# Optimization experiments

Measured on AMD Instinct MI355X. Metric: run time of the kernel, lower is better.

The kernel has to match this reference:

```python
import jax, jax.numpy as jnp
import numpy as np

DIM = 768
HEADS = 6
HD = DIM // HEADS
B, N = 8, 4096
EPS = 1e-12  # torch F.normalize default


def setup_inputs() -> dict:
    key = jax.random.key(0)
    k1, k2, k3, k4, k5 = jax.random.split(key, 5)
    x = jax.random.normal(k1, (B, N, DIM), dtype=jnp.float32)
    y = jax.random.normal(k2, (B, N, DIM), dtype=jnp.float32)
    W_qkv = jax.random.normal(k3, (DIM, 2 * DIM), dtype=jnp.float32) * (1.0 / np.sqrt(DIM))
    temperature = jnp.ones((HEADS, 1, 1), dtype=jnp.float32)
    W_proj = jax.random.normal(k4, (DIM, DIM), dtype=jnp.float32) * (1.0 / np.sqrt(DIM))
    b_proj = jax.random.normal(k5, (DIM,), dtype=jnp.float32) * 0.01
    return {"x": x, "y": y, "W_qkv": W_qkv, "temperature": temperature,
            "W_proj": W_proj, "b_proj": b_proj}


def _l2norm(t):
    # F.normalize(dim=-1): v / max(||v||, eps)
    n = jnp.sqrt(jnp.sum(t * t, axis=-1, keepdims=True))
    return t / jnp.maximum(n, EPS)


def reference(x, y, W_qkv, temperature, W_proj, b_proj):
    Bx, Nx, C = x.shape
    # qkv: [B,N,2C] -> [B,N,2,H,hd] -> q,k: [B,H,hd,N]
    qkv = (x @ W_qkv).reshape(Bx, Nx, 2, HEADS, HD)
    qkv = jnp.transpose(qkv, (2, 0, 3, 4, 1))  # [2,B,H,hd,N]
    q, k = qkv[0], qkv[1]
    # v: [B,H,hd,N]
    v = jnp.transpose(y.reshape(Bx, Nx, HEADS, HD), (0, 2, 3, 1))
    q = _l2norm(q)  # normalize over token dim N
    k = _l2norm(k)
    # channel-channel attention: [B,H,hd,hd]
    attn = jnp.einsum('bhcn,bhdn->bhcd', q, k) * temperature
    attn = jax.nn.softmax(attn, axis=-1)
    out = jnp.einsum('bhcd,bhdn->bhcn', attn, v)  # [B,H,hd,N]
    out = jnp.transpose(out, (0, 3, 1, 2)).reshape(Bx, Nx, C)
    return out @ W_proj + b_proj
```

## Files before the change

kernel.cpp:

```cpp
#include <hip/hip_runtime.h>
#include <hip/hip_bf16.h>

using bf16 = __hip_bfloat16;
typedef __attribute__((ext_vector_type(4))) float f32x4;
typedef __attribute__((ext_vector_type(8))) short bf16x8;

constexpr int Ntok   = 4096;
constexpr int Cdim   = 768;
constexpr int Hn     = 6;
constexpr int HD     = 128;
constexpr int QKcols = 1536;

#define AS1 __attribute__((address_space(1)))
#define AS3 __attribute__((address_space(3)))

__device__ inline void gload_lds16(const bf16* g, bf16* l) {
    __builtin_amdgcn_global_load_lds((const AS1 void*)g, (AS3 void*)l, 16, 0, 0);
}

__device__ inline int4 cvt8_f32_to_bf16(const float* p) {
    const float4 a0 = *reinterpret_cast<const float4*>(p);
    const float4 a1 = *reinterpret_cast<const float4*>(p + 4);
    union { int4 i; bf16 h[8]; } u;
    u.h[0] = __float2bfloat16(a0.x); u.h[1] = __float2bfloat16(a0.y);
    u.h[2] = __float2bfloat16(a0.z); u.h[3] = __float2bfloat16(a0.w);
    u.h[4] = __float2bfloat16(a1.x); u.h[5] = __float2bfloat16(a1.y);
    u.h[6] = __float2bfloat16(a1.z); u.h[7] = __float2bfloat16(a1.w);
    return u.i;
}

__global__ __launch_bounds__(256) void cvt_kernel(const float* __restrict__ in,
                                                  bf16* __restrict__ out) {
    const size_t i = ((size_t)blockIdx.x * 256 + threadIdx.x) * 8;
    *reinterpret_cast<int4*>(out + i) = cvt8_f32_to_bf16(in + i);
}

__global__ void transpose_kernel(const float* __restrict__ W, bf16* __restrict__ Wt,
                                 int K, int N) {
    __shared__ bf16 tile[32][33];
    const int n0 = blockIdx.x * 32, k0 = blockIdx.y * 32;
    const int tx = threadIdx.x, ty = threadIdx.y;
    for (int i = 0; i < 32; i += 8)
        tile[ty + i][tx] = __float2bfloat16(W[(size_t)(k0 + ty + i) * N + n0 + tx]);
    __syncthreads();
    for (int i = 0; i < 32; i += 8)
        Wt[(size_t)(n0 + ty + i) * K + k0 + tx] = tile[tx][ty + i];
}

template <bool C_F32, bool BIAS>
__global__ __launch_bounds__(256) void gemm_bt(const bf16* __restrict__ A,
                                               const bf16* __restrict__ Bt,
                                               const float* __restrict__ bias,
                                               void* __restrict__ Cv,
                                               int M, int N, int K, int bt_bstride) {
    __shared__ bf16 As[128 * 32];
    __shared__ bf16 Bs[128 * 32];

    const int m0   = blockIdx.y * 128, n0 = blockIdx.x * 128;
    Bt += (size_t)(m0 >> 12) * bt_bstride;
    const int tid  = threadIdx.x;
    const int wave = tid >> 6, lane = tid & 63;
    const int wq   = wave >> 1, wr = wave & 1;
    const int lm   = lane & 15, quad = lane >> 4;

    const int srow = tid >> 2, scol = (tid & 3) * 8;
    const bf16* Ag = A  + (size_t)(m0 + srow) * K + scol;
    const bf16* Bg = Bt + (size_t)(n0 + srow) * K + scol;
    bf16* Al0 = &As[srow * 32 + scol];
    bf16* Al1 = &As[(64 + srow) * 32 + scol];
    bf16* Bl0 = &Bs[srow * 32 + scol];
    bf16* Bl1 = &Bs[(64 + srow) * 32 + scol];

    f32x4 acc[4][4] = {};

    for (int k0 = 0; k0 < K; k0 += 32) {
        __syncthreads();
        gload_lds16(Ag + k0,                  Al0);
        gload_lds16(Ag + (size_t)64 * K + k0, Al1);
        gload_lds16(Bg + k0,                  Bl0);
        gload_lds16(Bg + (size_t)64 * K + k0, Bl1);
        __syncthreads();

        bf16x8 af[4], bfr[4];
#pragma unroll
        for (int t = 0; t < 4; t++) {
            af[t]  = *reinterpret_cast<const bf16x8*>(&As[(wq * 64 + t * 16 + lm) * 32 + quad * 8]);
            bfr[t] = *reinterpret_cast<const bf16x8*>(&Bs[(wr * 64 + t * 16 + lm) * 32 + quad * 8]);
        }
#pragma unroll
        for (int mt = 0; mt < 4; mt++)
#pragma unroll
            for (int nt = 0; nt < 4; nt++)
                acc[mt][nt] = __builtin_amdgcn_mfma_f32_16x16x32_bf16(af[mt], bfr[nt], acc[mt][nt], 0, 0, 0);
    }

    const int cm = m0 + wq * 64, cn = n0 + wr * 64;
#pragma unroll
    for (int mt = 0; mt < 4; mt++) {
#pragma unroll
        for (int nt = 0; nt < 4; nt++) {
            const int col = cn + nt * 16 + lm;
            const float bv = BIAS ? bias[col] : 0.0f;
#pragma unroll
            for (int r = 0; r < 4; r++) {
                const int row = cm + mt * 16 + quad * 4 + r;
                if constexpr (C_F32)
                    ((float*)Cv)[(size_t)row * N + col] = acc[mt][nt][r] + bv;
                else
                    ((bf16*)Cv)[(size_t)row * N + col] = __float2bfloat16(acc[mt][nt][r] + bv);
            }
        }
    }
}

__global__ __launch_bounds__(256) void gram_x_kernel(const bf16* __restrict__ xb,
                                                     bf16* __restrict__ G) {
    constexpr int BKn = 64;
    constexpr int LDT = BKn + 8;
    __shared__ bf16 Qt[HD * LDT];
    __shared__ bf16 Kt[HD * LDT];

    int ci = 0, rem = blockIdx.x, rowlen = 6;
    while (rem >= rowlen) { rem -= rowlen; rowlen--; ci++; }
    const int di = ci + rem;
    const int b = blockIdx.y;
    const int c0 = ci * 128, d0 = di * 128;

    const int tid = threadIdx.x, wave = tid >> 6, lane = tid & 63;
    const int lm = lane & 15, quad = lane >> 4;
    const size_t base = (size_t)b * Ntok * Cdim;

    f32x4 acc[2][8] = {};

    for (int n0 = 0; n0 < Ntok; n0 += BKn) {
        __syncthreads();
#pragma unroll
        for (int r = 0; r < 4; r++) {
            const int chunk = tid + 256 * r;
            const int nl = chunk & 63;
            const int j0 = (chunk >> 6) * 8;
            bf16 vq[8], vk[8];
            *reinterpret_cast<int4*>(vq) = *reinterpret_cast<const int4*>(xb + base + (size_t)(n0 + nl) * Cdim + c0 + j0);
            *reinterpret_cast<int4*>(vk) = *reinterpret_cast<const int4*>(xb + base + (size_t)(n0 + nl) * Cdim + d0 + j0);
#pragma unroll
            for (int u = 0; u < 8; u++) {
                Qt[(j0 + u) * LDT + nl] = vq[u];
                Kt[(j0 + u) * LDT + nl] = vk[u];
            }
        }
        __syncthreads();
#pragma unroll
        for (int ks = 0; ks < 2; ks++) {
            bf16x8 aq[2], bk[8];
#pragma unroll
            for (int mt = 0; mt < 2; mt++)
                aq[mt] = *reinterpret_cast<const bf16x8*>(&Qt[(wave * 32 + mt * 16 + lm) * LDT + ks * 32 + quad * 8]);
#pragma unroll
            for (int dt = 0; dt < 8; dt++)
                bk[dt] = *reinterpret_cast<const bf16x8*>(&Kt[(dt * 16 + lm) * LDT + ks * 32 + quad * 8]);
#pragma unroll
            for (int mt = 0; mt < 2; mt++)
#pragma unroll
                for (int dt = 0; dt < 8; dt++)
                    acc[mt][dt] = __builtin_amdgcn_mfma_f32_16x16x32_bf16(aq[mt], bk[dt], acc[mt][dt], 0, 0, 0);
        }
    }

    bf16* Gb = G + (size_t)b * Cdim * Cdim;
#pragma unroll
    for (int mt = 0; mt < 2; mt++)
#pragma unroll
        for (int dt = 0; dt < 8; dt++)
#pragma unroll
            for (int r = 0; r < 4; r++) {
                const int c = wave * 32 + mt * 16 + quad * 4 + r;
                const int d = dt * 16 + lm;
                const bf16 v = __float2bfloat16(acc[mt][dt][r]);
                Gb[(size_t)(c0 + c) * Cdim + d0 + d] = v;
                if (ci != di) Gb[(size_t)(d0 + d) * Cdim + c0 + c] = v;
            }
}

__global__ __launch_bounds__(256) void head_kernel(const bf16* __restrict__ GW,
                                                   const bf16* __restrict__ Wtq,
                                                   const bf16* __restrict__ Wtp,
                                                   const float* __restrict__ temp,
                                                   bf16* __restrict__ WeffT) {
    constexpr int LDT = 72;
    constexpr int LDP = 136;
    __shared__ bf16 Kt[HD * LDT];
    __shared__ bf16 At[HD * LDP];
    __shared__ float invq[HD], invk[HD];

    const int bh = blockIdx.x, b = bh / Hn, h = bh % Hn;
    const int tid = threadIdx.x, wave = tid >> 6, lane = tid & 63;
    const int lm = lane & 15, quad = lane >> 4;
    const int qoff = h * HD, koff = Cdim + h * HD;
    const float th = temp[h];

    {
        const int cl = tid & 127;
        const bool isk = tid >= 128;
        const int colg = (isk ? koff : qoff) + cl;
        const bf16* wt = Wtq + (size_t)colg * Cdim;
        const bf16* gw = GW + (size_t)b * Cdim * QKcols + colg;
        float s = 0.0f;
        for (int r = 0; r < Cdim; r += 8) {
            bf16 wv[8];
            *reinterpret_cast<int4*>(wv) = *reinterpret_cast<const int4*>(wt + r);
#pragma unroll
            for (int u = 0; u < 8; u++)
                s += (float)wv[u] * (float)gw[(size_t)(r + u) * QKcols];
        }
        (isk ? invk : invq)[cl] = 1.0f / fmaxf(sqrtf(fmaxf(s, 0.0f)), 1e-12f);
    }

    f32x4 acc[2][8] = {};
    const bf16* GWk = GW + (size_t)b * Cdim * QKcols + koff;
    for (int r0 = 0; r0 < Cdim; r0 += 64) {
        __syncthreads();
#pragma unroll
        for (int rr = 0; rr < 4; rr++) {
            const int chunk = tid + 256 * rr;
            const int rl = chunk & 63;
            const int j0 = (chunk >> 6) * 8;
            bf16 vk[8];
            *reinterpret_cast<int4*>(vk) = *reinterpret_cast<const int4*>(GWk + (size_t)(r0 + rl) * QKcols + j0);
#pragma unroll
            for (int u = 0; u < 8; u++)
                Kt[(j0 + u) * LDT + rl] = vk[u];
        }
        __syncthreads();
#pragma unroll
        for (int ks = 0; ks < 2; ks++) {
            bf16x8 aq[2], bk[8];
#pragma unroll
            for (int mt = 0; mt < 2; mt++)
                aq[mt] = *reinterpret_cast<const bf16x8*>(Wtq + (size_t)(qoff + wave * 32 + mt * 16 + lm) * Cdim + r0 + ks * 32 + quad * 8);
#pragma unroll
            for (int dt = 0; dt < 8; dt++)
                bk[dt] = *reinterpret_cast<const bf16x8*>(&Kt[(dt * 16 + lm) * LDT + ks * 32 + quad * 8]);
#pragma unroll
            for (int mt = 0; mt < 2; mt++)
#pragma unroll
                for (int dt = 0; dt < 8; dt++)
                    acc[mt][dt] = __builtin_amdgcn_mfma_f32_16x16x32_bf16(aq[mt], bk[dt], acc[mt][dt], 0, 0, 0);
        }
    }

    __syncthreads();
    float ikv[8];
#pragma unroll
    for (int dt = 0; dt < 8; dt++) ikv[dt] = invk[dt * 16 + lm] * th;
#pragma unroll
    for (int mt = 0; mt < 2; mt++) {
#pragma unroll
        for (int r = 0; r < 4; r++) {
            const int c = wave * 32 + mt * 16 + quad * 4 + r;
            const float iq = invq[c];
            float v[8], m = -1e30f;
#pragma unroll
            for (int dt = 0; dt < 8; dt++) { v[dt] = acc[mt][dt][r] * iq * ikv[dt]; m = fmaxf(m, v[dt]); }
            m = fmaxf(m, __shfl_xor(m, 1, 64));
            m = fmaxf(m, __shfl_xor(m, 2, 64));
            m = fmaxf(m, __shfl_xor(m, 4, 64));
            m = fmaxf(m, __shfl_xor(m, 8, 64));
            float sum = 0.0f;
#pragma unroll
            for (int dt = 0; dt < 8; dt++) { v[dt] = __expf(v[dt] - m); sum += v[dt]; }
            sum += __shfl_xor(sum, 1, 64);
            sum += __shfl_xor(sum, 2, 64);
            sum += __shfl_xor(sum, 4, 64);
            sum += __shfl_xor(sum, 8, 64);
            const float inv = 1.0f / sum;
#pragma unroll
            for (int dt = 0; dt < 8; dt++)
                At[(dt * 16 + lm) * LDP + c] = __float2bfloat16(v[dt] * inv);
        }
    }
    __syncthreads();

    bf16* Wo = WeffT + (size_t)b * Cdim * Cdim + h * HD;
    for (int jo = 0; jo < Cdim; jo += 256) {
        const int jb = jo + wave * 64;
        f32x4 a2[4][8] = {};
#pragma unroll
        for (int ks = 0; ks < 4; ks++) {
            bf16x8 aw[4], bp[8];
#pragma unroll
            for (int mt = 0; mt < 4; mt++)
                aw[mt] = *reinterpret_cast<const bf16x8*>(Wtp + (size_t)(jb + mt * 16 + lm) * Cdim + h * HD + ks * 32 + quad * 8);
#pragma unroll
            for (int dt = 0; dt < 8; dt++)
                bp[dt] = *reinterpret_cast<const bf16x8*>(&At[(dt * 16 + lm) * LDP + ks * 32 + quad * 8]);
#pragma unroll
            for (int mt = 0; mt < 4; mt++)
#pragma unroll
                for (int dt = 0; dt < 8; dt++)
                    a2[mt][dt] = __builtin_amdgcn_mfma_f32_16x16x32_bf16(aw[mt], bp[dt], a2[mt][dt], 0, 0, 0);
        }
#pragma unroll
        for (int mt = 0; mt < 4; mt++)
#pragma unroll
            for (int dt = 0; dt < 8; dt++)
#pragma unroll
                for (int r = 0; r < 4; r++)
                    Wo[(size_t)(jb + mt * 16 + quad * 4 + r) * Cdim + dt * 16 + lm] =
                        __float2bfloat16(a2[mt][dt][r]);
    }
}

extern "C" void kernel_launch(void* const* d_in, const int* in_sizes, int n_in,
                              void* d_out, int out_size, void* d_ws, size_t ws_size,
                              hipStream_t stream) {
    const float* x     = (const float*)d_in[0];
    const float* y     = (const float*)d_in[1];
    const float* Wqkv  = (const float*)d_in[2];
    const float* temp  = (const float*)d_in[3];
    const float* Wproj = (const float*)d_in[4];
    const float* bproj = (const float*)d_in[5];
    float* out = (float*)d_out;

    char* ws = (char*)d_ws;
    size_t o = 0;
    bf16* xb      = (bf16*)(ws + o); o += (size_t)32768 * 768 * 2;
    bf16* yb      = (bf16*)(ws + o); o += (size_t)32768 * 768 * 2;
    bf16* G       = (bf16*)(ws + o); o += (size_t)8 * 768 * 768 * 2;
    bf16* GW      = (bf16*)(ws + o); o += (size_t)8 * 768 * 1536 * 2;
    bf16* WeffT   = (bf16*)(ws + o); o += (size_t)8 * 768 * 768 * 2;
    bf16* Wt_qkv  = (bf16*)(ws + o); o += (size_t)1536 * 768 * 2;
    bf16* Wt_proj = (bf16*)(ws + o); o += (size_t)768 * 768 * 2;

    dim3 tb(32, 8);
    transpose_kernel<<<dim3(1536 / 32, 768 / 32), tb, 0, stream>>>(Wqkv, Wt_qkv, 768, 1536);
    transpose_kernel<<<dim3(768 / 32, 768 / 32), tb, 0, stream>>>(Wproj, Wt_proj, 768, 768);

    cvt_kernel<<<12288, 256, 0, stream>>>(x, xb);
    cvt_kernel<<<12288, 256, 0, stream>>>(y, yb);

    gram_x_kernel<<<dim3(21, 8), 256, 0, stream>>>(xb, G);

    gemm_bt<false, false><<<dim3(1536 / 128, 6144 / 128), 256, 0, stream>>>(
        G, Wt_qkv, nullptr, GW, 6144, 1536, 768, 0);

    head_kernel<<<48, 256, 0, stream>>>(GW, Wt_qkv, Wt_proj, temp, WeffT);

    gemm_bt<true, true><<<dim3(768 / 128, 32768 / 128), 256, 0, stream>>>(
        yb, WeffT, bproj, out, 32768, 768, 768, 768 * 768);
}
```

Baseline: 566.6 us.

## Split-K Gram with transposed x, and separate diag, head and fold kernels

x is now transposed to bf16 [C,N] so the Gram matrix can use the direct-to-LDS gemm path. Its K dimension is split four ways into fp32 partials with a separate reduce kernel, which raises occupancy above the previous 168 blocks. GW is computed transposed through a batched gemm. The norm diagonal, the head attention and the W_proj fold move into separate, more parallel kernels (the fold now runs on 288 blocks instead of 48). This adds extra launches and partial-buffer traffic.

```diff
diff --git a/kernel.cpp b/kernel.cpp
--- a/kernel.cpp
+++ b/kernel.cpp
@@ -10,6 +10,8 @@
 constexpr int Hn     = 6;
 constexpr int HD     = 128;
 constexpr int QKcols = 1536;
+constexpr int NTRI   = 21;
+constexpr int SPLITK = 4;
 
 #define AS1 __attribute__((address_space(1)))
 #define AS3 __attribute__((address_space(3)))
@@ -47,17 +49,37 @@
         Wt[(size_t)(n0 + ty + i) * K + k0 + tx] = tile[tx][ty + i];
 }
 
+__global__ __launch_bounds__(256) void transpose_x(const float* __restrict__ x,
+                                                   bf16* __restrict__ xT) {
+    __shared__ bf16 tile[64][34];
+    const int b = blockIdx.z, n0 = blockIdx.y * 64, c0 = blockIdx.x * 32;
+    const int tid = threadIdx.x;
+    const int c_r = tid & 31, n_r = tid >> 5;
+    const float* xp = x + ((size_t)b * Ntok + n0) * Cdim + c0;
+#pragma unroll
+    for (int i = 0; i < 64; i += 8)
+        tile[n_r + i][c_r] = __float2bfloat16(xp[(size_t)(n_r + i) * Cdim + c_r]);
+    __syncthreads();
+    const int n_w = tid & 63, c_w = tid >> 6;
+    bf16* op = xT + ((size_t)b * Cdim + c0) * Ntok + n0;
+#pragma unroll
+    for (int i = 0; i < 32; i += 4)
+        op[(size_t)(c_w + i) * Ntok + n_w] = tile[n_w][c_w + i];
+}
+
 template <bool C_F32, bool BIAS>
 __global__ __launch_bounds__(256) void gemm_bt(const bf16* __restrict__ A,
                                                const bf16* __restrict__ Bt,
                                                const float* __restrict__ bias,
                                                void* __restrict__ Cv,
-                                               int M, int N, int K, int bt_bstride) {
+                                               int N, int K,
+                                               size_t a_bs, size_t bt_bs, size_t c_bs) {
     __shared__ bf16 As[128 * 32];
     __shared__ bf16 Bs[128 * 32];
 
+    A  += (size_t)blockIdx.z * a_bs;
+    Bt += (size_t)blockIdx.z * bt_bs;
     const int m0   = blockIdx.y * 128, n0 = blockIdx.x * 128;
-    Bt += (size_t)(m0 >> 12) * bt_bstride;
     const int tid  = threadIdx.x;
     const int wave = tid >> 6, lane = tid & 63;
     const int wq   = wave >> 1, wr = wave & 1;
@@ -105,150 +127,160 @@
             for (int r = 0; r < 4; r++) {
                 const int row = cm + mt * 16 + quad * 4 + r;
                 if constexpr (C_F32)
-                    ((float*)Cv)[(size_t)row * N + col] = acc[mt][nt][r] + bv;
+                    ((float*)Cv + (size_t)blockIdx.z * c_bs)[(size_t)row * N + col] = acc[mt][nt][r] + bv;
                 else
-                    ((bf16*)Cv)[(size_t)row * N + col] = __float2bfloat16(acc[mt][nt][r] + bv);
+                    ((bf16*)Cv + (size_t)blockIdx.z * c_bs)[(size_t)row * N + col] = __float2bfloat16(acc[mt][nt][r] + bv);
             }
         }
     }
 }
 
-__global__ __launch_bounds__(256) void gram_x_kernel(const bf16* __restrict__ xb,
-                                                     bf16* __restrict__ G) {
-    constexpr int BKn = 64;
-    constexpr int LDT = BKn + 8;
-    __shared__ bf16 Qt[HD * LDT];
-    __shared__ bf16 Kt[HD * LDT];
+__global__ __launch_bounds__(256) void gram_k(const bf16* __restrict__ xT,
+                                              float* __restrict__ partial) {
+    __shared__ bf16 As[128 * 32];
+    __shared__ bf16 Bs[128 * 32];
 
     int ci = 0, rem = blockIdx.x, rowlen = 6;
     while (rem >= rowlen) { rem -= rowlen; rowlen--; ci++; }
     const int di = ci + rem;
+    const int b = blockIdx.y, s = blockIdx.z;
+    const int c0 = ci * 128, d0 = di * 128;
+
+    const int tid  = threadIdx.x;
+    const int wave = tid >> 6, lane = tid & 63;
+    const int wq   = wave >> 1, wr = wave & 1;
+    const int lm   = lane & 15, quad = lane >> 4;
+
+    const int srow = tid >> 2, scol = (tid & 3) * 8;
+    const size_t base = (size_t)b * Cdim * Ntok + (size_t)s * (Ntok / SPLITK);
+    const bf16* Ag = xT + base + (size_t)(c0 + srow) * Ntok + scol;
+    const bf16* Bg = xT + base + (size_t)(d0 + srow) * Ntok + scol;
+    bf16* Al0 = &As[srow * 32 + scol];
+    bf16* Al1 = &As[(64 + srow) * 32 + scol];
+    bf16* Bl0 = &Bs[srow * 32 + scol];
+    bf16* Bl1 = &Bs[(64 + srow) * 32 + scol];
+
+    f32x4 acc[4][4] = {};
+
+    for (int k0 = 0; k0 < Ntok / SPLITK; k0 += 32) {
+        __syncthreads();
+        gload_lds16(Ag + k0,                     Al0);
+        gload_lds16(Ag + (size_t)64 * Ntok + k0, Al1);
+        gload_lds16(Bg + k0,                     Bl0);
+        gload_lds16(Bg + (size_t)64 * Ntok + k0, Bl1);
+        __syncthreads();
+
+        bf16x8 af[4], bfr[4];
+#pragma unroll
+        for (int t = 0; t < 4; t++) {
+            af[t]  = *reinterpret_cast<const bf16x8*>(&As[(wq * 64 + t * 16 + lm) * 32 + quad * 8]);
+            bfr[t] = *reinterpret_cast<const bf16x8*>(&Bs[(wr * 64 + t * 16 + lm) * 32 + quad * 8]);
+        }
+#pragma unroll
+        for (int mt = 0; mt < 4; mt++)
+#pragma unroll
+            for (int nt = 0; nt < 4; nt++)
+                acc[mt][nt] = __builtin_amdgcn_mfma_f32_16x16x32_bf16(af[mt], bfr[nt], acc[mt][nt], 0, 0, 0);
+    }
+
+    float* pp = partial + (((size_t)blockIdx.x * 8 + b) * SPLITK + s) * 16384;
+#pragma unroll
+    for (int mt = 0; mt < 4; mt++)
+#pragma unroll
+        for (int nt = 0; nt < 4; nt++)
+#pragma unroll
+            for (int r = 0; r < 4; r++)
+                pp[(size_t)(wq * 64 + mt * 16 + quad * 4 + r) * 128 + wr * 64 + nt * 16 + lm] = acc[mt][nt][r];
+}
+
+__global__ __launch_bounds__(256) void gram_reduce(const float* __restrict__ partial,
+                                                   bf16* __restrict__ G) {
+    int ci = 0, rem = blockIdx.x, rowlen = 6;
+    while (rem >= rowlen) { rem -= rowlen; rowlen--; ci++; }
+    const int di = ci + rem, b = blockIdx.y;
+    const int c0 = ci * 128, d0 = di * 128;
+    const float* p0 = partial + ((size_t)blockIdx.x * 8 + b) * SPLITK * 16384;
+    bf16* Gb = G + (size_t)b * Cdim * Cdim;
+    const int tid = threadIdx.x;
+
+    for (int i = 0; i < 16; i++) {
+        const int off = i * 1024 + tid * 4;
+        float4 v = *reinterpret_cast<const float4*>(p0 + off);
+#pragma unroll
+        for (int s2 = 1; s2 < SPLITK; s2++) {
+            const float4 u = *reinterpret_cast<const float4*>(p0 + (size_t)s2 * 16384 + off);
+            v.x += u.x; v.y += u.y; v.z += u.z; v.w += u.w;
+        }
+        const int c = off >> 7, d = off & 127;
+        union { uint2 u2; bf16 h[4]; } pk;
+        pk.h[0] = __float2bfloat16(v.x); pk.h[1] = __float2bfloat16(v.y);
+        pk.h[2] = __float2bfloat16(v.z); pk.h[3] = __float2bfloat16(v.w);
+        *reinterpret_cast<uint2*>(&Gb[(size_t)(c0 + c) * Cdim + d0 + d]) = pk.u2;
+        if (ci != di) {
+#pragma unroll
+            for (int jj = 0; jj < 4; jj++)
+                Gb[(size_t)(d0 + d + jj) * Cdim + c0 + c] = pk.h[jj];
+        }
+    }
+}
+
+__global__ __launch_bounds__(256) void diag_kernel(const bf16* __restrict__ Wtq,
+                                                   const bf16* __restrict__ GWT,
+                                                   float* __restrict__ invn) {
     const int b = blockIdx.y;
-    const int c0 = ci * 128, d0 = di * 128;
-
-    const int tid = threadIdx.x, wave = tid >> 6, lane = tid & 63;
-    const int lm = lane & 15, quad = lane >> 4;
-    const size_t base = (size_t)b * Ntok * Cdim;
-
-    f32x4 acc[2][8] = {};
-
-    for (int n0 = 0; n0 < Ntok; n0 += BKn) {
-        __syncthreads();
-#pragma unroll
-        for (int r = 0; r < 4; r++) {
-            const int chunk = tid + 256 * r;
-            const int nl = chunk & 63;
-            const int j0 = (chunk >> 6) * 8;
-            bf16 vq[8], vk[8];
-            *reinterpret_cast<int4*>(vq) = *reinterpret_cast<const int4*>(xb + base + (size_t)(n0 + nl) * Cdim + c0 + j0);
-            *reinterpret_cast<int4*>(vk) = *reinterpret_cast<const int4*>(xb + base + (size_t)(n0 + nl) * Cdim + d0 + j0);
-#pragma unroll
-            for (int u = 0; u < 8; u++) {
-                Qt[(j0 + u) * LDT + nl] = vq[u];
-                Kt[(j0 + u) * LDT + nl] = vk[u];
-            }
-        }
-        __syncthreads();
-#pragma unroll
-        for (int ks = 0; ks < 2; ks++) {
-            bf16x8 aq[2], bk[8];
-#pragma unroll
-            for (int mt = 0; mt < 2; mt++)
-                aq[mt] = *reinterpret_cast<const bf16x8*>(&Qt[(wave * 32 + mt * 16 + lm) * LDT + ks * 32 + quad * 8]);
-#pragma unroll
-            for (int dt = 0; dt < 8; dt++)
-                bk[dt] = *reinterpret_cast<const bf16x8*>(&Kt[(dt * 16 + lm) * LDT + ks * 32 + quad * 8]);
-#pragma unroll
-            for (int mt = 0; mt < 2; mt++)
-#pragma unroll
-                for (int dt = 0; dt < 8; dt++)
-                    acc[mt][dt] = __builtin_amdgcn_mfma_f32_16x16x32_bf16(aq[mt], bk[dt], acc[mt][dt], 0, 0, 0);
-        }
-    }
-
-    bf16* Gb = G + (size_t)b * Cdim * Cdim;
-#pragma unroll
-    for (int mt = 0; mt < 2; mt++)
-#pragma unroll
-        for (int dt = 0; dt < 8; dt++)
-#pragma unroll
-            for (int r = 0; r < 4; r++) {
-                const int c = wave * 32 + mt * 16 + quad * 4 + r;
-                const int d = dt * 16 + lm;
-                const bf16 v = __float2bfloat16(acc[mt][dt][r]);
-                Gb[(size_t)(c0 + c) * Cdim + d0 + d] = v;
-                if (ci != di) Gb[(size_t)(d0 + d) * Cdim + c0 + c] = v;
-            }
-}
-
-__global__ __launch_bounds__(256) void head_kernel(const bf16* __restrict__ GW,
+    const int col = blockIdx.x * 32 + (threadIdx.x >> 3);
+    const int sub = threadIdx.x & 7;
+    const bf16* w = Wtq + (size_t)col * Cdim + sub * 8;
+    const bf16* g = GWT + ((size_t)b * QKcols + col) * Cdim + sub * 8;
+    float s = 0.0f;
+    for (int i = 0; i < 12; i++) {
+        bf16 wv[8], gv[8];
+        *reinterpret_cast<int4*>(wv) = *reinterpret_cast<const int4*>(w + i * 64);
+        *reinterpret_cast<int4*>(gv) = *reinterpret_cast<const int4*>(g + i * 64);
+#pragma unroll
+        for (int u = 0; u < 8; u++) s += (float)wv[u] * (float)gv[u];
+    }
+    s += __shfl_xor(s, 1, 64);
+    s += __shfl_xor(s, 2, 64);
+    s += __shfl_xor(s, 4, 64);
+    if (sub == 0)
+        invn[(size_t)b * QKcols + col] = 1.0f / fmaxf(sqrtf(fmaxf(s, 0.0f)), 1e-12f);
+}
+
+__global__ __launch_bounds__(256) void head_kernel(const bf16* __restrict__ GWT,
                                                    const bf16* __restrict__ Wtq,
-                                                   const bf16* __restrict__ Wtp,
+                                                   const float* __restrict__ invn,
                                                    const float* __restrict__ temp,
-                                                   bf16* __restrict__ WeffT) {
-    constexpr int LDT = 72;
+                                                   bf16* __restrict__ attnT) {
     constexpr int LDP = 136;
-    __shared__ bf16 Kt[HD * LDT];
     __shared__ bf16 At[HD * LDP];
-    __shared__ float invq[HD], invk[HD];
 
     const int bh = blockIdx.x, b = bh / Hn, h = bh % Hn;
     const int tid = threadIdx.x, wave = tid >> 6, lane = tid & 63;
     const int lm = lane & 15, quad = lane >> 4;
     const int qoff = h * HD, koff = Cdim + h * HD;
     const float th = temp[h];
-
-    {
-        const int cl = tid & 127;
-        const bool isk = tid >= 128;
-        const int colg = (isk ? koff : qoff) + cl;
-        const bf16* wt = Wtq + (size_t)colg * Cdim;
-        const bf16* gw = GW + (size_t)b * Cdim * QKcols + colg;
-        float s = 0.0f;
-        for (int r = 0; r < Cdim; r += 8) {
-            bf16 wv[8];
-            *reinterpret_cast<int4*>(wv) = *reinterpret_cast<const int4*>(wt + r);
-#pragma unroll
-            for (int u = 0; u < 8; u++)
-                s += (float)wv[u] * (float)gw[(size_t)(r + u) * QKcols];
-        }
-        (isk ? invk : invq)[cl] = 1.0f / fmaxf(sqrtf(fmaxf(s, 0.0f)), 1e-12f);
-    }
+    const float* invq = invn + (size_t)b * QKcols + qoff;
+    const float* invk = invn + (size_t)b * QKcols + koff;
 
     f32x4 acc[2][8] = {};
-    const bf16* GWk = GW + (size_t)b * Cdim * QKcols + koff;
-    for (int r0 = 0; r0 < Cdim; r0 += 64) {
-        __syncthreads();
-#pragma unroll
-        for (int rr = 0; rr < 4; rr++) {
-            const int chunk = tid + 256 * rr;
-            const int rl = chunk & 63;
-            const int j0 = (chunk >> 6) * 8;
-            bf16 vk[8];
-            *reinterpret_cast<int4*>(vk) = *reinterpret_cast<const int4*>(GWk + (size_t)(r0 + rl) * QKcols + j0);
-#pragma unroll
-            for (int u = 0; u < 8; u++)
-                Kt[(j0 + u) * LDT + rl] = vk[u];
-        }
-        __syncthreads();
-#pragma unroll
-        for (int ks = 0; ks < 2; ks++) {
-            bf16x8 aq[2], bk[8];
-#pragma unroll
-            for (int mt = 0; mt < 2; mt++)
-                aq[mt] = *reinterpret_cast<const bf16x8*>(Wtq + (size_t)(qoff + wave * 32 + mt * 16 + lm) * Cdim + r0 + ks * 32 + quad * 8);
+    const bf16* Aq = Wtq + (size_t)(qoff + wave * 32 + lm) * Cdim + quad * 8;
+    const bf16* Bk = GWT + ((size_t)b * QKcols + koff + lm) * Cdim + quad * 8;
+    for (int r0 = 0; r0 < Cdim; r0 += 32) {
+        bf16x8 aq[2], bk[8];
+#pragma unroll
+        for (int mt = 0; mt < 2; mt++)
+            aq[mt] = *reinterpret_cast<const bf16x8*>(Aq + (size_t)mt * 16 * Cdim + r0);
+#pragma unroll
+        for (int dt = 0; dt < 8; dt++)
+            bk[dt] = *reinterpret_cast<const bf16x8*>(Bk + (size_t)dt * 16 * Cdim + r0);
+#pragma unroll
+        for (int mt = 0; mt < 2; mt++)
 #pragma unroll
             for (int dt = 0; dt < 8; dt++)
-                bk[dt] = *reinterpret_cast<const bf16x8*>(&Kt[(dt * 16 + lm) * LDT + ks * 32 + quad * 8]);
-#pragma unroll
-            for (int mt = 0; mt < 2; mt++)
-#pragma unroll
-                for (int dt = 0; dt < 8; dt++)
-                    acc[mt][dt] = __builtin_amdgcn_mfma_f32_16x16x32_bf16(aq[mt], bk[dt], acc[mt][dt], 0, 0, 0);
-        }
-    }
-
-    __syncthreads();
+                acc[mt][dt] = __builtin_amdgcn_mfma_f32_16x16x32_bf16(aq[mt], bk[dt], acc[mt][dt], 0, 0, 0);
+    }
+
     float ikv[8];
 #pragma unroll
     for (int dt = 0; dt < 8; dt++) ikv[dt] = invk[dt * 16 + lm] * th;
@@ -280,34 +312,50 @@
     }
     __syncthreads();
 
+#pragma unroll
+    for (int i = 0; i < 8; i++) {
+        const int idx = tid + 256 * i;
+        const int d = idx >> 4, c8 = (idx & 15) * 8;
+        const bf16x8 v = *reinterpret_cast<const bf16x8*>(&At[d * LDP + c8]);
+        *reinterpret_cast<bf16x8*>(&attnT[((size_t)bh * HD + d) * HD + c8]) = v;
+    }
+}
+
+__global__ __launch_bounds__(256) void fold_kernel(const bf16* __restrict__ attnT,
+                                                   const bf16* __restrict__ Wtp,
+                                                   bf16* __restrict__ WeffT) {
+    const int j0 = blockIdx.x * 128, bh = blockIdx.y, b = bh / Hn, h = bh % Hn;
+    const int tid = threadIdx.x, wave = tid >> 6, lane = tid & 63;
+    const int lm = lane & 15, quad = lane >> 4;
+
+    f32x4 acc[2][8] = {};
+    const bf16* Ap = Wtp + (size_t)(j0 + wave * 32 + lm) * Cdim + h * HD + quad * 8;
+    const bf16* Bd = attnT + ((size_t)bh * HD + lm) * HD + quad * 8;
+#pragma unroll
+    for (int ks = 0; ks < HD; ks += 32) {
+        bf16x8 aw[2], bd[8];
+#pragma unroll
+        for (int mt = 0; mt < 2; mt++)
+            aw[mt] = *reinterpret_cast<const bf16x8*>(Ap + (size_t)mt * 16 * Cdim + ks);
+#pragma unroll
+        for (int dt = 0; dt < 8; dt++)
+            bd[dt] = *reinterpret_cast<const bf16x8*>(Bd + (size_t)dt * 16 * HD + ks);
+#pragma unroll
+        for (int mt = 0; mt < 2; mt++)
+#pragma unroll
+            for (int dt = 0; dt < 8; dt++)
+                acc[mt][dt] = __builtin_amdgcn_mfma_f32_16x16x32_bf16(aw[mt], bd[dt], acc[mt][dt], 0, 0, 0);
+    }
+
     bf16* Wo = WeffT + (size_t)b * Cdim * Cdim + h * HD;
-    for (int jo = 0; jo < Cdim; jo += 256) {
-        const int jb = jo + wave * 64;
-        f32x4 a2[4][8] = {};
-#pragma unroll
-        for (int ks = 0; ks < 4; ks++) {
-            bf16x8 aw[4], bp[8];
-#pragma unroll
-            for (int mt = 0; mt < 4; mt++)
-                aw[mt] = *reinterpret_cast<const bf16x8*>(Wtp + (size_t)(jb + mt * 16 + lm) * Cdim + h * HD + ks * 32 + quad * 8);
-#pragma unroll
-            for (int dt = 0; dt < 8; dt++)
-                bp[dt] = *reinterpret_cast<const bf16x8*>(&At[(dt * 16 + lm) * LDP + ks * 32 + quad * 8]);
-#pragma unroll
-            for (int mt = 0; mt < 4; mt++)
-#pragma unroll
-                for (int dt = 0; dt < 8; dt++)
-                    a2[mt][dt] = __builtin_amdgcn_mfma_f32_16x16x32_bf16(aw[mt], bp[dt], a2[mt][dt], 0, 0, 0);
-        }
-#pragma unroll
-        for (int mt = 0; mt < 4; mt++)
-#pragma unroll
-            for (int dt = 0; dt < 8; dt++)
-#pragma unroll
-                for (int r = 0; r < 4; r++)
-                    Wo[(size_t)(jb + mt * 16 + quad * 4 + r) * Cdim + dt * 16 + lm] =
-                        __float2bfloat16(a2[mt][dt][r]);
-    }
+#pragma unroll
+    for (int mt = 0; mt < 2; mt++)
+#pragma unroll
+        for (int dt = 0; dt < 8; dt++)
+#pragma unroll
+            for (int r = 0; r < 4; r++)
+                Wo[(size_t)(j0 + wave * 32 + mt * 16 + quad * 4 + r) * Cdim + dt * 16 + lm] =
+                    __float2bfloat16(acc[mt][dt][r]);
 }
 
 extern "C" void kernel_launch(void* const* d_in, const int* in_sizes, int n_in,
@@ -323,28 +371,36 @@
 
     char* ws = (char*)d_ws;
     size_t o = 0;
-    bf16* xb      = (bf16*)(ws + o); o += (size_t)32768 * 768 * 2;
-    bf16* yb      = (bf16*)(ws + o); o += (size_t)32768 * 768 * 2;
-    bf16* G       = (bf16*)(ws + o); o += (size_t)8 * 768 * 768 * 2;
-    bf16* GW      = (bf16*)(ws + o); o += (size_t)8 * 768 * 1536 * 2;
-    bf16* WeffT   = (bf16*)(ws + o); o += (size_t)8 * 768 * 768 * 2;
-    bf16* Wt_qkv  = (bf16*)(ws + o); o += (size_t)1536 * 768 * 2;
-    bf16* Wt_proj = (bf16*)(ws + o); o += (size_t)768 * 768 * 2;
+    bf16*  xT      = (bf16*)(ws + o); o += (size_t)8 * Cdim * Ntok * 2;
+    bf16*  yb      = (bf16*)(ws + o); o += (size_t)8 * Ntok * Cdim * 2;
+    float* partial = (float*)(ws + o); o += (size_t)NTRI * 8 * SPLITK * 16384 * 4;
+    bf16*  G       = (bf16*)(ws + o); o += (size_t)8 * Cdim * Cdim * 2;
+    bf16*  GWT     = (bf16*)(ws + o); o += (size_t)8 * QKcols * Cdim * 2;
+    bf16*  WeffT   = (bf16*)(ws + o); o += (size_t)8 * Cdim * Cdim * 2;
+    bf16*  Wt_qkv  = (bf16*)(ws + o); o += (size_t)QKcols * Cdim * 2;
+    bf16*  Wt_proj = (bf16*)(ws + o); o += (size_t)Cdim * Cdim * 2;
+    float* invn    = (float*)(ws + o); o += (size_t)8 * QKcols * 4;
+    bf16*  attnT   = (bf16*)(ws + o); o += (size_t)48 * HD * HD * 2;
 
     dim3 tb(32, 8);
-    transpose_kernel<<<dim3(1536 / 32, 768 / 32), tb, 0, stream>>>(Wqkv, Wt_qkv, 768, 1536);
-    transpose_kernel<<<dim3(768 / 32, 768 / 32), tb, 0, stream>>>(Wproj, Wt_proj, 768, 768);
-
-    cvt_kernel<<<12288, 256, 0, stream>>>(x, xb);
+    transpose_kernel<<<dim3(QKcols / 32, Cdim / 32), tb, 0, stream>>>(Wqkv, Wt_qkv, Cdim, QKcols);
+    transpose_kernel<<<dim3(Cdim / 32, Cdim / 32), tb, 0, stream>>>(Wproj, Wt_proj, Cdim, Cdim);
+
+    transpose_x<<<dim3(Cdim / 32, Ntok / 64, 8), 256, 0, stream>>>(x, xT);
     cvt_kernel<<<12288, 256, 0, stream>>>(y, yb);
 
-    gram_x_kernel<<<dim3(21, 8), 256, 0, stream>>>(xb, G);
-
-    gemm_bt<false, false><<<dim3(1536 / 128, 6144 / 128), 256, 0, stream>>>(
-        G, Wt_qkv, nullptr, GW, 6144, 1536, 768, 0);
-
-    head_kernel<<<48, 256, 0, stream>>>(GW, Wt_qkv, Wt_proj, temp, WeffT);
-
-    gemm_bt<true, true><<<dim3(768 / 128, 32768 / 128), 256, 0, stream>>>(
-        yb, WeffT, bproj, out, 32768, 768, 768, 768 * 768);
-}
+    gram_k<<<dim3(NTRI, 8, SPLITK), 256, 0, stream>>>(xT, partial);
+    gram_reduce<<<dim3(NTRI, 8), 256, 0, stream>>>(partial, G);
+
+    gemm_bt<false, false><<<dim3(Cdim / 128, QKcols / 128, 8), 256, 0, stream>>>(
+        Wt_qkv, G, nullptr, GWT, Cdim, Cdim,
+        0, (size_t)Cdim * Cdim, (size_t)QKcols * Cdim);
+
+    diag_kernel<<<dim3(QKcols / 32, 8), 256, 0, stream>>>(Wt_qkv, GWT, invn);
+    head_kernel<<<48, 256, 0, stream>>>(GWT, Wt_qkv, invn, temp, attnT);
+    fold_kernel<<<dim3(Cdim / 128, 48), 256, 0, stream>>>(attnT, Wt_proj, WeffT);
+
+    gemm_bt<true, true><<<dim3(Cdim / 128, Ntok / 128, 8), 256, 0, stream>>>(
+        yb, WeffT, bproj, out, Cdim, Cdim,
+        (size_t)Ntok * Cdim, (size_t)Cdim * Cdim, (size_t)Ntok * Cdim);
+}
```

After: 489.4 us. -13.6%, faster.
